# Optimization experiments

Measured on AMD Instinct MI355X. Metric: run time of the kernel, lower is better.

Reference implementation:

```python
import jax, jax.numpy as jnp
import numpy as np
from jax import lax

# Hyperparameters (match init_kwargs)
A = 0.9          # dynamic model: x_t = A * x_{t-1} + SIGMA * eps
SIGMA = 1.0
OBS_SIGMA = 1.0
LR = 0.1
ALPHA = 0.9
ITERATIONS = 3
EPS = 1e-8


def _pairwise_sq(x):
    # (B,N,N) squared euclidean distances ||x_i - x_j||^2
    x2 = jnp.sum(x * x, -1)
    sq = x2[:, :, None] + x2[:, None, :] - 2.0 * jnp.einsum('bid,bjd->bij', x, x)
    return jnp.maximum(sq, 0.0)


def _log_dynamic(x, prev):
    # logd[b,i,j] = log N(x_i ; A*prev_j, SIGMA^2 I)
    D = x.shape[-1]
    x2 = jnp.sum(x * x, -1)
    p2 = jnp.sum(prev * prev, -1)
    sq = x2[:, :, None] - 2.0 * A * jnp.einsum('bid,bjd->bij', x, prev) + (A * A) * p2[:, None, :]
    return -0.5 * sq / (SIGMA ** 2) - 0.5 * D * jnp.log(2.0 * jnp.pi * SIGMA ** 2)


def _post_grad(x, prev, obs):
    # softmax over j == max-subtract / exp / weighted-mean of d_log_dynamic in the original
    w = jax.nn.softmax(_log_dynamic(x, prev), axis=-1)                 # (B,N,N)
    mean_prev = jnp.einsum('bij,bjd->bid', w, prev)                    # sum_j w_ij * prev_j
    dyn_grad = -(x - A * mean_prev) / (SIGMA ** 2)                     # = sum_j w_ij * d_log_dynamic
    obs_grad = -(x - obs[:, None, :]) / (OBS_SIGMA ** 2)               # observation_model.d_score
    return dyn_grad + obs_grad


def _svgd(x, grad_fn):
    B, N, D = x.shape
    logN = jnp.log(jnp.asarray(N, x.dtype))
    step = jnp.zeros_like(x)
    for _ in range(ITERATIONS):
        sq = _pairwise_sq(x)                                           # (B,N,N)
        flat = jnp.sqrt(sq).reshape(B, N * N)
        med = jnp.sort(flat, axis=-1)[:, (N * N - 1) // 2]             # torch lower median of cdist
        h = (med * med / logN)[:, None, None]                          # (B,1,1) bandwidth
        rbf = jnp.exp(-sq / h)                                         # exp(-(1/h)*||x_i-x_j||^2)
        g = grad_fn(x)                                                 # (B,N,D) posterior score at particles
        kxy = jnp.einsum('bij,bjd->bid', rbf, g)                       # sum_j rbf_ij * g_j
        # sum_j d_rbf_ij = (2/h) * (x_i * sum_j rbf_ij - sum_j rbf_ij * x_j)   (avoids (B,N,N,D))
        rep = (2.0 / h) * (x * jnp.sum(rbf, -1)[..., None] - jnp.einsum('bij,bjd->bid', rbf, x))
        stein = (kxy + rep) / N
        step = ALPHA * step + (1.0 - ALPHA) * stein * stein            # RMSprop accumulator
        x = x + LR * stein / (jnp.sqrt(step) + EPS)
    return x


def setup_inputs() -> dict:
    key = jax.random.key(0)
    k1, k2, k3 = jax.random.split(key, 3)
    B, N, D = 8, 2048, 4
    return {
        'prev_state': jax.random.normal(k1, (B, N, D), jnp.float32),
        'observation': jax.random.normal(k2, (B, D), jnp.float32),
        'noise': jax.random.normal(k3, (B, N, D), jnp.float32),
    }


def reference(prev_state, observation, noise):
    N = prev_state.shape[1]
    logN = jnp.log(jnp.asarray(N, prev_state.dtype))
    # dynamic_model.sample
    state = A * prev_state + SIGMA * noise
    # post: logsumexp over i (dim=-2) of log_dynamic[b,i,j]
    log_post = jax.nn.logsumexp(_log_dynamic(state, prev_state), axis=1)   # (B,N)
    new_state = lax.stop_gradient(_svgd(state, lambda x: _post_grad(x, prev_state, observation)))
    log_weight = log_post - lax.stop_gradient(log_post) - logN             # value == -log N
    return jnp.concatenate([new_state, log_weight[..., None]], axis=-1)    # (B,N,D+1)
```

## Files before the change

### kernel.cpp

```cpp
#include <hip/hip_runtime.h>
#include <math.h>


#define NPART 2048
#define KRANK 2097151
#define LOGN_F 7.6246189861593985f
#define A_C 0.9f

__global__ __launch_bounds__(256) void k_init(const float* __restrict__ prev,
                                              const float* __restrict__ noise,
                                              float* __restrict__ x0,
                                              float* __restrict__ apb,
                                              int* __restrict__ hist0) {
  int idx = blockIdx.x * 256 + threadIdx.x;
  float4 p  = ((const float4*)prev)[idx];
  float4 nz = ((const float4*)noise)[idx];
  float4 ap = make_float4(A_C*p.x, A_C*p.y, A_C*p.z, A_C*p.w);
  ((float4*)x0)[idx]  = make_float4(ap.x+nz.x, ap.y+nz.y, ap.z+nz.z, ap.w+nz.w);
  ((float4*)apb)[idx] = ap;
  if (idx < 4096) ((int4*)hist0)[idx] = make_int4(0, 0, 0, 0);
}

__global__ __launch_bounds__(256) void k_s1(const float* __restrict__ x,
                                            const float* __restrict__ apb,
                                            const float* __restrict__ obs,
                                            float* __restrict__ g,
                                            int* __restrict__ hist0,
                                            int* __restrict__ hist1) {
  if (threadIdx.x < 4)
    ((int4*)hist1)[blockIdx.x*4 + threadIdx.x] = make_int4(0, 0, 0, 0);

  if (blockIdx.x < 1024) {
    int b   = blockIdx.x >> 7;
    int ip  = threadIdx.x >> 4;
    int sub = threadIdx.x & 15;
    int i = (blockIdx.x & 127)*16 + ip;
    const float4* ab = (const float4*)apb + b*NPART;
    float4 xi = ((const float4*)x)[b*NPART + i];

    float sum1 = 0.f, sum2 = 0.f;
    float4 acc1 = make_float4(0.f,0.f,0.f,0.f);
    float4 acc2 = make_float4(0.f,0.f,0.f,0.f);
#pragma unroll 4
    for (int c = 0; c < 64; ++c) {
      int j = sub + 16*c;
      float4 a1 = ab[j];
      float4 a2 = ab[j + 1024];
      float dx1 = xi.x-a1.x, dy1 = xi.y-a1.y, dz1 = xi.z-a1.z, dw1 = xi.w-a1.w;
      float dx2 = xi.x-a2.x, dy2 = xi.y-a2.y, dz2 = xi.z-a2.z, dw2 = xi.w-a2.w;
      float e1 = __expf(-0.5f*(dx1*dx1 + dy1*dy1 + dz1*dz1 + dw1*dw1));
      float e2 = __expf(-0.5f*(dx2*dx2 + dy2*dy2 + dz2*dz2 + dw2*dw2));
      sum1 += e1; sum2 += e2;
      acc1.x += e1*a1.x; acc1.y += e1*a1.y; acc1.z += e1*a1.z; acc1.w += e1*a1.w;
      acc2.x += e2*a2.x; acc2.y += e2*a2.y; acc2.z += e2*a2.z; acc2.w += e2*a2.w;
    }
    float sum = sum1 + sum2;
    float4 acc = make_float4(acc1.x+acc2.x, acc1.y+acc2.y,
                             acc1.z+acc2.z, acc1.w+acc2.w);
#pragma unroll
    for (int d = 1; d < 16; d <<= 1) {
      sum   += __shfl_xor(sum, d);
      acc.x += __shfl_xor(acc.x, d);
      acc.y += __shfl_xor(acc.y, d);
      acc.z += __shfl_xor(acc.z, d);
      acc.w += __shfl_xor(acc.w, d);
    }
    if (sub == 0) {
      float inv = 1.0f / sum;
      float4 ob = ((const float4*)obs)[b];
      float4 gg;
      gg.x = acc.x*inv + ob.x - 2.0f*xi.x;
      gg.y = acc.y*inv + ob.y - 2.0f*xi.y;
      gg.z = acc.z*inv + ob.z - 2.0f*xi.z;
      gg.w = acc.w*inv + ob.w - 2.0f*xi.w;
      ((float4*)g)[b*NPART + i] = gg;
    }
  } else {
    int bid   = blockIdx.x - 1024;
    int b     = bid >> 7;
    int sub2  = bid & 127;
    int itile = sub2 >> 4;
    int ktile = sub2 & 15;
    __shared__ float4 sxi[256];
    __shared__ float4 sxw[320];
    __shared__ int    sh[2*2049];

    const float4* xb = (const float4*)x + b*NPART;
    int ibase = itile*256;
    int k0 = ktile*64 + 1;
    sxi[threadIdx.x] = xb[ibase + threadIdx.x];
    for (int t = threadIdx.x; t < 320; t += 256)
      sxw[t] = xb[(ibase + k0 + t) & (NPART - 1)];
    for (int t = threadIdx.x; t < 2*2049; t += 256) sh[t] = 0;
    __syncthreads();

    float4 xi = sxi[threadIdx.x];
    int cofs = (threadIdx.x & 1) * 2049;
#pragma unroll 4
    for (int kk = 0; kk < 64; ++kk) {
      int w = (ktile == 15 && kk == 63) ? 1 : 2;
      float4 xj = sxw[threadIdx.x + kk];
      float dx = xi.x - xj.x, dy = xi.y - xj.y;
      float dz = xi.z - xj.z, dw = xi.w - xj.w;
      float sq = dx*dx + dy*dy + dz*dz + dw*dw;
      atomicAdd(&sh[cofs + (__float_as_uint(sq) >> 20)], w);
    }
    __syncthreads();
    int* hb = hist0 + b*2048;
    for (int t = threadIdx.x; t < 2048; t += 256) {
      int c = sh[t] + sh[t + 2049];
      if (c) atomicAdd(&hb[t], c);
    }
  }
}

__global__ __launch_bounds__(256) void k_s2(const float* __restrict__ x,
                                            int* __restrict__ state,
                                            const int* __restrict__ hist0,
                                            int* __restrict__ hist1) {
  int b     = blockIdx.x >> 7;
  int sub2  = blockIdx.x & 127;
  int itile = sub2 >> 4;
  int ktile = sub2 & 15;
  __shared__ float4 sxi[256];
  __shared__ float4 sxw[320];
  __shared__ int    sh[4096];
  __shared__ int    part[256];
  __shared__ int    s_sel0;

  const float4* xb = (const float4*)x + b*NPART;
  int ibase = itile*256;
  int k0 = ktile*64 + 1;
  sxi[threadIdx.x] = xb[ibase + threadIdx.x];
  for (int t = threadIdx.x; t < 320; t += 256)
    sxw[t] = xb[(ibase + k0 + t) & (NPART - 1)];
  for (int t = threadIdx.x; t < 4096; t += 256) sh[t] = 0;

  const int* h0 = hist0 + b*2048;
  int4 c0 = ((const int4*)h0)[threadIdx.x*2];
  int4 c1 = ((const int4*)h0)[threadIdx.x*2 + 1];
  int s = c0.x+c0.y+c0.z+c0.w + c1.x+c1.y+c1.z+c1.w;
  if (threadIdx.x == 0) s += NPART;
  part[threadIdx.x] = s;
  __syncthreads();
  if (threadIdx.x == 0) {
    int r = KRANK, cum = 0, ch = 0;
    for (; ch < 256; ++ch) { if (cum + part[ch] > r) break; cum += part[ch]; }
    int4 d0 = ((const int4*)h0)[ch*2];
    int4 d1 = ((const int4*)h0)[ch*2 + 1];
    int cc[8] = {d0.x,d0.y,d0.z,d0.w,d1.x,d1.y,d1.z,d1.w};
    if (ch == 0) cc[0] += NPART;
    int q = 0;
    for (;; ++q) { if (cum + cc[q] > r) break; cum += cc[q]; }
    int bin = ch*8 + q;
    s_sel0 = bin;
    if (sub2 == 0) { state[b*2] = bin; state[b*2 + 1] = r - cum; }
  }
  __syncthreads();
  int sel0 = s_sel0;

  float4 xi = sxi[threadIdx.x];
#pragma unroll 4
  for (int kk = 0; kk < 64; ++kk) {
    int w = (ktile == 15 && kk == 63) ? 1 : 2;
    float4 xj = sxw[threadIdx.x + kk];
    float dx = xi.x - xj.x, dy = xi.y - xj.y;
    float dz = xi.z - xj.z, dw = xi.w - xj.w;
    float sq = dx*dx + dy*dy + dz*dz + dw*dw;
    unsigned bits = __float_as_uint(sq);
    if ((int)(bits >> 20) == sel0) atomicAdd(&sh[(bits >> 8) & 4095], w);
  }
  __syncthreads();
  int* hb = hist1 + b*4096;
  for (int t = threadIdx.x; t < 4096; t += 256) {
    int c = sh[t];
    if (c) atomicAdd(&hb[t], c);
  }
}

template <int MODE>
__global__ __launch_bounds__(256) void k_s3(const float* __restrict__ x,
                                            const float* __restrict__ g,
                                            const int* __restrict__ state,
                                            int* __restrict__ hist0,
                                            const int* __restrict__ hist1,
                                            float* __restrict__ stepb,
                                            float* __restrict__ xout,
                                            float* __restrict__ outp) {
  if (threadIdx.x < 8)
    ((int4*)hist0)[blockIdx.x*8 + threadIdx.x] = make_int4(0, 0, 0, 0);

  int b   = blockIdx.x >> 6;
  int blk = blockIdx.x & 63;
  __shared__ int   part[256];
  __shared__ float shp[2];

  const int* h1 = hist1 + b*4096;
  int4 c0 = ((const int4*)h1)[threadIdx.x*4 + 0];
  int4 c1 = ((const int4*)h1)[threadIdx.x*4 + 1];
  int4 c2 = ((const int4*)h1)[threadIdx.x*4 + 2];
  int4 c3 = ((const int4*)h1)[threadIdx.x*4 + 3];
  int s = c0.x+c0.y+c0.z+c0.w + c1.x+c1.y+c1.z+c1.w
        + c2.x+c2.y+c2.z+c2.w + c3.x+c3.y+c3.z+c3.w;
  int sel0 = state[b*2];
  if (threadIdx.x == 0 && sel0 == 0) s += NPART;
  part[threadIdx.x] = s;
  __syncthreads();
  if (threadIdx.x == 0) {
    int r = state[b*2 + 1], cum = 0, ch = 0;
    for (; ch < 256; ++ch) { if (cum + part[ch] > r) break; cum += part[ch]; }
    int4 d0 = ((const int4*)h1)[ch*4 + 0];
    int4 d1 = ((const int4*)h1)[ch*4 + 1];
    int4 d2 = ((const int4*)h1)[ch*4 + 2];
    int4 d3 = ((const int4*)h1)[ch*4 + 3];
    int cc[16] = {d0.x,d0.y,d0.z,d0.w, d1.x,d1.y,d1.z,d1.w,
                  d2.x,d2.y,d2.z,d2.w, d3.x,d3.y,d3.z,d3.w};
    if (sel0 == 0 && ch == 0) cc[0] += NPART;
    int q = 0;
    for (;; ++q) { if (cum + cc[q] > r) break; cum += cc[q]; }
    int bin = ch*16 + q;
    unsigned mb = (((unsigned)sel0) << 20) | (((unsigned)bin) << 8) | 128u;
    float med = sqrtf(__uint_as_float(mb));
    float h = med * med / LOGN_F;
    shp[0] = -1.0f / h;
    shp[1] =  2.0f / h;
  }
  __syncthreads();
  float neginvh = shp[0];
  float two_h   = shp[1];

  int ip  = threadIdx.x >> 4;
  int sub = threadIdx.x & 15;
  int rowA = blk*32 + ip;
  int rowB = rowA + 16;
  const float4* xb = (const float4*)x + b*NPART;
  const float4* gb = (const float4*)g + b*NPART;
  float4 xiA = xb[rowA];
  float4 xiB = xb[rowB];

  float4 SdA = make_float4(0.f,0.f,0.f,0.f), SgA = SdA;
  float4 SdB = SdA, SgB = SdA;
#pragma unroll 4
  for (int c = 0; c < 128; ++c) {
    int j = sub + 16*c;
    float4 xj = xb[j];
    float4 gj = gb[j];
    float dxA = xiA.x-xj.x, dyA = xiA.y-xj.y, dzA = xiA.z-xj.z, dwA = xiA.w-xj.w;
    float dxB = xiB.x-xj.x, dyB = xiB.y-xj.y, dzB = xiB.z-xj.z, dwB = xiB.w-xj.w;
    float eA = __expf((dxA*dxA + dyA*dyA + dzA*dzA + dwA*dwA) * neginvh);
    float eB = __expf((dxB*dxB + dyB*dyB + dzB*dzB + dwB*dwB) * neginvh);
    SdA.x += eA*dxA; SdA.y += eA*dyA; SdA.z += eA*dzA; SdA.w += eA*dwA;
    SdB.x += eB*dxB; SdB.y += eB*dyB; SdB.z += eB*dzB; SdB.w += eB*dwB;
    SgA.x += eA*gj.x; SgA.y += eA*gj.y; SgA.z += eA*gj.z; SgA.w += eA*gj.w;
    SgB.x += eB*gj.x; SgB.y += eB*gj.y; SgB.z += eB*gj.z; SgB.w += eB*gj.w;
  }
#pragma unroll
  for (int d = 1; d < 16; d <<= 1) {
    SdA.x += __shfl_xor(SdA.x, d); SdA.y += __shfl_xor(SdA.y, d);
    SdA.z += __shfl_xor(SdA.z, d); SdA.w += __shfl_xor(SdA.w, d);
    SgA.x += __shfl_xor(SgA.x, d); SgA.y += __shfl_xor(SgA.y, d);
    SgA.z += __shfl_xor(SgA.z, d); SgA.w += __shfl_xor(SgA.w, d);
    SdB.x += __shfl_xor(SdB.x, d); SdB.y += __shfl_xor(SdB.y, d);
    SdB.z += __shfl_xor(SdB.z, d); SdB.w += __shfl_xor(SdB.w, d);
    SgB.x += __shfl_xor(SgB.x, d); SgB.y += __shfl_xor(SgB.y, d);
    SgB.z += __shfl_xor(SgB.z, d); SgB.w += __shfl_xor(SgB.w, d);
  }
  if (sub == 0) {
    const float invN = 1.0f / 2048.0f;
#pragma unroll
    for (int rr = 0; rr < 2; ++rr) {
      int row = rr ? rowB : rowA;
      float4 xi = rr ? xiB : xiA;
      float4 Sd = rr ? SdB : SdA;
      float4 Sg = rr ? SgB : SgA;
      float4 sv;
      sv.x = (Sg.x + two_h*Sd.x) * invN;
      sv.y = (Sg.y + two_h*Sd.y) * invN;
      sv.z = (Sg.z + two_h*Sd.z) * invN;
      sv.w = (Sg.w + two_h*Sd.w) * invN;
      float4 st;
      if (MODE == 0) {
        st = make_float4(0.1f*sv.x*sv.x, 0.1f*sv.y*sv.y,
                         0.1f*sv.z*sv.z, 0.1f*sv.w*sv.w);
      } else {
        st = ((float4*)stepb)[b*NPART + row];
        st.x = 0.9f*st.x + 0.1f*sv.x*sv.x;
        st.y = 0.9f*st.y + 0.1f*sv.y*sv.y;
        st.z = 0.9f*st.z + 0.1f*sv.z*sv.z;
        st.w = 0.9f*st.w + 0.1f*sv.w*sv.w;
      }
      float4 xn;
      xn.x = xi.x + 0.1f*sv.x / (sqrtf(st.x) + 1e-8f);
      xn.y = xi.y + 0.1f*sv.y / (sqrtf(st.y) + 1e-8f);
      xn.z = xi.z + 0.1f*sv.z / (sqrtf(st.z) + 1e-8f);
      xn.w = xi.w + 0.1f*sv.w / (sqrtf(st.w) + 1e-8f);
      if (MODE != 2) {
        ((float4*)stepb)[b*NPART + row] = st;
        ((float4*)xout)[b*NPART + row] = xn;
      } else {
        float* o = outp + (size_t)(b*NPART + row) * 5;
        o[0] = xn.x; o[1] = xn.y; o[2] = xn.z; o[3] = xn.w;
        o[4] = -LOGN_F;
      }
    }
  }
}

extern "C" void kernel_launch(void* const* d_in, const int* in_sizes, int n_in,
                              void* d_out, int out_size, void* d_ws, size_t ws_size,
                              hipStream_t stream) {
  const float* prev  = (const float*)d_in[0];
  const float* obs   = (const float*)d_in[1];
  const float* noise = (const float*)d_in[2];
  float* out = (float*)d_out;

  float* ws = (float*)d_ws;
  float* xA    = ws;
  float* xB    = xA + 65536;
  float* gbuf  = xB + 65536;
  float* stepb = gbuf + 65536;
  float* apb   = stepb + 65536;
  int*   state = (int*)(apb + 65536);
  int*   hist0 = state + 16;
  int*   hist1 = hist0 + 8*2048;

  k_init<<<64, 256, 0, stream>>>(prev, noise, xA, apb, hist0);

  float* xc = xA;
  float* xn = xB;
  for (int it = 0; it < 3; ++it) {
    k_s1<<<2048, 256, 0, stream>>>(xc, apb, obs, gbuf, hist0, hist1);
    k_s2<<<1024, 256, 0, stream>>>(xc, state, hist0, hist1);
    if (it == 0) {
      k_s3<0><<<512, 256, 0, stream>>>(xc, gbuf, state, hist0, hist1, stepb, xn, nullptr);
    } else if (it == 1) {
      k_s3<1><<<512, 256, 0, stream>>>(xc, gbuf, state, hist0, hist1, stepb, xn, nullptr);
    } else {
      k_s3<2><<<512, 256, 0, stream>>>(xc, gbuf, state, hist0, hist1, stepb, nullptr, out);
    }
    float* t = xc; xc = xn; xn = t;
  }
}
```

Measured before the change: 359.5 us.

## Register-block four rows per wavefront in gradient and Stein kernels, interleave block roles

The gradient part of k_s1 and the Stein kernel k_s3 now give each 64-lane wavefront four particle rows and stride across all 2048 j values, so every loaded j particle is reused for four rows. k_s3 folds the repulsive term into a precomputed per-j coefficient (g_j - (2/h) x_j) plus a row-sum term, which removes per-pair multiply-adds. k_s1 interleaves its gradient and histogram blocks by blockIdx parity, and k_s3 launches 1024 blocks. The histogram zeroing is redistributed (init clears all three histograms), and occupancy hints are added in exchange for more registers per thread and longer 64-wide shuffle reductions.

```diff
diff --git a/kernel.cpp b/kernel.cpp
--- a/kernel.cpp
+++ b/kernel.cpp
@@ -11,74 +11,115 @@
                                               const float* __restrict__ noise,
                                               float* __restrict__ x0,
                                               float* __restrict__ apb,
-                                              int* __restrict__ hist0) {
+                                              int* __restrict__ hists) {
   int idx = blockIdx.x * 256 + threadIdx.x;
   float4 p  = ((const float4*)prev)[idx];
   float4 nz = ((const float4*)noise)[idx];
   float4 ap = make_float4(A_C*p.x, A_C*p.y, A_C*p.z, A_C*p.w);
   ((float4*)x0)[idx]  = make_float4(ap.x+nz.x, ap.y+nz.y, ap.z+nz.z, ap.w+nz.w);
   ((float4*)apb)[idx] = ap;
-  if (idx < 4096) ((int4*)hist0)[idx] = make_int4(0, 0, 0, 0);
-}
-
-__global__ __launch_bounds__(256) void k_s1(const float* __restrict__ x,
-                                            const float* __restrict__ apb,
-                                            const float* __restrict__ obs,
-                                            float* __restrict__ g,
-                                            int* __restrict__ hist0,
-                                            int* __restrict__ hist1) {
+  if (idx < 12288) ((int4*)hists)[idx] = make_int4(0, 0, 0, 0);
+}
+
+__device__ __forceinline__ void grad_j(const float4* xi, const float4 ap,
+                                       float* s, float4* acc) {
+#pragma unroll
+  for (int r = 0; r < 4; ++r) {
+    float dx = xi[r].x - ap.x, dy = xi[r].y - ap.y;
+    float dz = xi[r].z - ap.z, dw = xi[r].w - ap.w;
+    float sq = fmaf(dx, dx, fmaf(dy, dy, fmaf(dz, dz, dw*dw)));
+    float e = __expf(-0.5f * sq);
+    s[r] += e;
+    acc[r].x = fmaf(e, ap.x, acc[r].x);
+    acc[r].y = fmaf(e, ap.y, acc[r].y);
+    acc[r].z = fmaf(e, ap.z, acc[r].z);
+    acc[r].w = fmaf(e, ap.w, acc[r].w);
+  }
+}
+
+__device__ __forceinline__ void stein_j(const float4* xi, const float4 xj,
+                                        const float4 gj, float two_h,
+                                        float ninvh, float* s0, float4* sc) {
+  float4 cj;
+  cj.x = fmaf(-two_h, xj.x, gj.x);
+  cj.y = fmaf(-two_h, xj.y, gj.y);
+  cj.z = fmaf(-two_h, xj.z, gj.z);
+  cj.w = fmaf(-two_h, xj.w, gj.w);
+#pragma unroll
+  for (int r = 0; r < 4; ++r) {
+    float dx = xi[r].x - xj.x, dy = xi[r].y - xj.y;
+    float dz = xi[r].z - xj.z, dw = xi[r].w - xj.w;
+    float sq = fmaf(dx, dx, fmaf(dy, dy, fmaf(dz, dz, dw*dw)));
+    float e = __expf(sq * ninvh);
+    s0[r] += e;
+    sc[r].x = fmaf(e, cj.x, sc[r].x);
+    sc[r].y = fmaf(e, cj.y, sc[r].y);
+    sc[r].z = fmaf(e, cj.z, sc[r].z);
+    sc[r].w = fmaf(e, cj.w, sc[r].w);
+  }
+}
+
+__global__ __launch_bounds__(256, 4) void k_s1(const float* __restrict__ x,
+                                               const float* __restrict__ apb,
+                                               const float* __restrict__ obs,
+                                               float* __restrict__ g,
+                                               int* __restrict__ hist0,
+                                               int* __restrict__ hist1) {
   if (threadIdx.x < 4)
     ((int4*)hist1)[blockIdx.x*4 + threadIdx.x] = make_int4(0, 0, 0, 0);
-
-  if (blockIdx.x < 1024) {
-    int b   = blockIdx.x >> 7;
-    int ip  = threadIdx.x >> 4;
-    int sub = threadIdx.x & 15;
-    int i = (blockIdx.x & 127)*16 + ip;
+  int role = blockIdx.x & 1;
+  int id   = blockIdx.x >> 1;
+
+  if (role == 0) {
+    int b = id >> 7;
+    int rbase = (id & 127)*16 + (threadIdx.x >> 6)*4;
+    int lane = threadIdx.x & 63;
+    const float4* xb = (const float4*)x + b*NPART;
     const float4* ab = (const float4*)apb + b*NPART;
-    float4 xi = ((const float4*)x)[b*NPART + i];
-
-    float sum1 = 0.f, sum2 = 0.f;
-    float4 acc1 = make_float4(0.f,0.f,0.f,0.f);
-    float4 acc2 = make_float4(0.f,0.f,0.f,0.f);
-#pragma unroll 4
-    for (int c = 0; c < 64; ++c) {
-      int j = sub + 16*c;
-      float4 a1 = ab[j];
-      float4 a2 = ab[j + 1024];
-      float dx1 = xi.x-a1.x, dy1 = xi.y-a1.y, dz1 = xi.z-a1.z, dw1 = xi.w-a1.w;
-      float dx2 = xi.x-a2.x, dy2 = xi.y-a2.y, dz2 = xi.z-a2.z, dw2 = xi.w-a2.w;
-      float e1 = __expf(-0.5f*(dx1*dx1 + dy1*dy1 + dz1*dz1 + dw1*dw1));
-      float e2 = __expf(-0.5f*(dx2*dx2 + dy2*dy2 + dz2*dz2 + dw2*dw2));
-      sum1 += e1; sum2 += e2;
-      acc1.x += e1*a1.x; acc1.y += e1*a1.y; acc1.z += e1*a1.z; acc1.w += e1*a1.w;
-      acc2.x += e2*a2.x; acc2.y += e2*a2.y; acc2.z += e2*a2.z; acc2.w += e2*a2.w;
-    }
-    float sum = sum1 + sum2;
-    float4 acc = make_float4(acc1.x+acc2.x, acc1.y+acc2.y,
-                             acc1.z+acc2.z, acc1.w+acc2.w);
-#pragma unroll
-    for (int d = 1; d < 16; d <<= 1) {
-      sum   += __shfl_xor(sum, d);
-      acc.x += __shfl_xor(acc.x, d);
-      acc.y += __shfl_xor(acc.y, d);
-      acc.z += __shfl_xor(acc.z, d);
-      acc.w += __shfl_xor(acc.w, d);
-    }
-    if (sub == 0) {
-      float inv = 1.0f / sum;
+    float4 xi[4];
+#pragma unroll
+    for (int r = 0; r < 4; ++r) xi[r] = xb[rbase + r];
+    float  sum[4] = {0.f, 0.f, 0.f, 0.f};
+    float4 acc[4] = {{0,0,0,0},{0,0,0,0},{0,0,0,0},{0,0,0,0}};
+
+    for (int c = 0; c < 2048; c += 256) {
+      int j = lane + c;
+      float4 aA = ab[j];
+      float4 aB = ab[j + 64];
+      float4 aC = ab[j + 128];
+      float4 aD = ab[j + 192];
+      grad_j(xi, aA, sum, acc);
+      grad_j(xi, aB, sum, acc);
+      grad_j(xi, aC, sum, acc);
+      grad_j(xi, aD, sum, acc);
+    }
+#pragma unroll
+    for (int d = 1; d < 64; d <<= 1) {
+#pragma unroll
+      for (int r = 0; r < 4; ++r) {
+        sum[r]   += __shfl_xor(sum[r], d);
+        acc[r].x += __shfl_xor(acc[r].x, d);
+        acc[r].y += __shfl_xor(acc[r].y, d);
+        acc[r].z += __shfl_xor(acc[r].z, d);
+        acc[r].w += __shfl_xor(acc[r].w, d);
+      }
+    }
+    if (lane == 0) {
       float4 ob = ((const float4*)obs)[b];
-      float4 gg;
-      gg.x = acc.x*inv + ob.x - 2.0f*xi.x;
-      gg.y = acc.y*inv + ob.y - 2.0f*xi.y;
-      gg.z = acc.z*inv + ob.z - 2.0f*xi.z;
-      gg.w = acc.w*inv + ob.w - 2.0f*xi.w;
-      ((float4*)g)[b*NPART + i] = gg;
+#pragma unroll
+      for (int r = 0; r < 4; ++r) {
+        float inv = 1.0f / sum[r];
+        float4 gg;
+        gg.x = fmaf(acc[r].x, inv, fmaf(-2.0f, xi[r].x, ob.x));
+        gg.y = fmaf(acc[r].y, inv, fmaf(-2.0f, xi[r].y, ob.y));
+        gg.z = fmaf(acc[r].z, inv, fmaf(-2.0f, xi[r].z, ob.z));
+        gg.w = fmaf(acc[r].w, inv, fmaf(-2.0f, xi[r].w, ob.w));
+        ((float4*)g)[b*NPART + rbase + r] = gg;
+      }
     }
   } else {
-    int bid   = blockIdx.x - 1024;
-    int b     = bid >> 7;
-    int sub2  = bid & 127;
+    int b     = id >> 7;
+    int sub2  = id & 127;
     int itile = sub2 >> 4;
     int ktile = sub2 & 15;
     __shared__ float4 sxi[256];
@@ -179,19 +220,18 @@
 }
 
 template <int MODE>
-__global__ __launch_bounds__(256) void k_s3(const float* __restrict__ x,
-                                            const float* __restrict__ g,
-                                            const int* __restrict__ state,
-                                            int* __restrict__ hist0,
-                                            const int* __restrict__ hist1,
-                                            float* __restrict__ stepb,
-                                            float* __restrict__ xout,
-                                            float* __restrict__ outp) {
-  if (threadIdx.x < 8)
-    ((int4*)hist0)[blockIdx.x*8 + threadIdx.x] = make_int4(0, 0, 0, 0);
-
-  int b   = blockIdx.x >> 6;
-  int blk = blockIdx.x & 63;
+__global__ __launch_bounds__(256, 4) void k_s3(const float* __restrict__ x,
+                                               const float* __restrict__ g,
+                                               const int* __restrict__ state,
+                                               int* __restrict__ hist0,
+                                               const int* __restrict__ hist1,
+                                               float* __restrict__ stepb,
+                                               float* __restrict__ xout,
+                                               float* __restrict__ outp) {
+  if (threadIdx.x < 4)
+    ((int4*)hist0)[blockIdx.x*4 + threadIdx.x] = make_int4(0, 0, 0, 0);
+
+  int b = blockIdx.x >> 7;
   __shared__ int   part[256];
   __shared__ float shp[2];
 
@@ -229,55 +269,49 @@
   float neginvh = shp[0];
   float two_h   = shp[1];
 
-  int ip  = threadIdx.x >> 4;
-  int sub = threadIdx.x & 15;
-  int rowA = blk*32 + ip;
-  int rowB = rowA + 16;
+  int rbase = (blockIdx.x & 127)*16 + (threadIdx.x >> 6)*4;
+  int lane = threadIdx.x & 63;
   const float4* xb = (const float4*)x + b*NPART;
   const float4* gb = (const float4*)g + b*NPART;
-  float4 xiA = xb[rowA];
-  float4 xiB = xb[rowB];
-
-  float4 SdA = make_float4(0.f,0.f,0.f,0.f), SgA = SdA;
-  float4 SdB = SdA, SgB = SdA;
-#pragma unroll 4
-  for (int c = 0; c < 128; ++c) {
-    int j = sub + 16*c;
-    float4 xj = xb[j];
-    float4 gj = gb[j];
-    float dxA = xiA.x-xj.x, dyA = xiA.y-xj.y, dzA = xiA.z-xj.z, dwA = xiA.w-xj.w;
-    float dxB = xiB.x-xj.x, dyB = xiB.y-xj.y, dzB = xiB.z-xj.z, dwB = xiB.w-xj.w;
-    float eA = __expf((dxA*dxA + dyA*dyA + dzA*dzA + dwA*dwA) * neginvh);
-    float eB = __expf((dxB*dxB + dyB*dyB + dzB*dzB + dwB*dwB) * neginvh);
-    SdA.x += eA*dxA; SdA.y += eA*dyA; SdA.z += eA*dzA; SdA.w += eA*dwA;
-    SdB.x += eB*dxB; SdB.y += eB*dyB; SdB.z += eB*dzB; SdB.w += eB*dwB;
-    SgA.x += eA*gj.x; SgA.y += eA*gj.y; SgA.z += eA*gj.z; SgA.w += eA*gj.w;
-    SgB.x += eB*gj.x; SgB.y += eB*gj.y; SgB.z += eB*gj.z; SgB.w += eB*gj.w;
-  }
-#pragma unroll
-  for (int d = 1; d < 16; d <<= 1) {
-    SdA.x += __shfl_xor(SdA.x, d); SdA.y += __shfl_xor(SdA.y, d);
-    SdA.z += __shfl_xor(SdA.z, d); SdA.w += __shfl_xor(SdA.w, d);
-    SgA.x += __shfl_xor(SgA.x, d); SgA.y += __shfl_xor(SgA.y, d);
-    SgA.z += __shfl_xor(SgA.z, d); SgA.w += __shfl_xor(SgA.w, d);
-    SdB.x += __shfl_xor(SdB.x, d); SdB.y += __shfl_xor(SdB.y, d);
-    SdB.z += __shfl_xor(SdB.z, d); SdB.w += __shfl_xor(SdB.w, d);
-    SgB.x += __shfl_xor(SgB.x, d); SgB.y += __shfl_xor(SgB.y, d);
-    SgB.z += __shfl_xor(SgB.z, d); SgB.w += __shfl_xor(SgB.w, d);
-  }
-  if (sub == 0) {
+  float4 xi[4];
+#pragma unroll
+  for (int r = 0; r < 4; ++r) xi[r] = xb[rbase + r];
+  float  S0[4] = {0.f, 0.f, 0.f, 0.f};
+  float4 Sc[4] = {{0,0,0,0},{0,0,0,0},{0,0,0,0},{0,0,0,0}};
+
+  for (int c = 0; c < 2048; c += 256) {
+    int j = lane + c;
+    float4 xjA = xb[j];        float4 gjA = gb[j];
+    float4 xjB = xb[j + 64];   float4 gjB = gb[j + 64];
+    float4 xjC = xb[j + 128];  float4 gjC = gb[j + 128];
+    float4 xjD = xb[j + 192];  float4 gjD = gb[j + 192];
+    stein_j(xi, xjA, gjA, two_h, neginvh, S0, Sc);
+    stein_j(xi, xjB, gjB, two_h, neginvh, S0, Sc);
+    stein_j(xi, xjC, gjC, two_h, neginvh, S0, Sc);
+    stein_j(xi, xjD, gjD, two_h, neginvh, S0, Sc);
+  }
+#pragma unroll
+  for (int d = 1; d < 64; d <<= 1) {
+#pragma unroll
+    for (int r = 0; r < 4; ++r) {
+      S0[r]   += __shfl_xor(S0[r], d);
+      Sc[r].x += __shfl_xor(Sc[r].x, d);
+      Sc[r].y += __shfl_xor(Sc[r].y, d);
+      Sc[r].z += __shfl_xor(Sc[r].z, d);
+      Sc[r].w += __shfl_xor(Sc[r].w, d);
+    }
+  }
+  if (lane == 0) {
     const float invN = 1.0f / 2048.0f;
 #pragma unroll
-    for (int rr = 0; rr < 2; ++rr) {
-      int row = rr ? rowB : rowA;
-      float4 xi = rr ? xiB : xiA;
-      float4 Sd = rr ? SdB : SdA;
-      float4 Sg = rr ? SgB : SgA;
+    for (int r = 0; r < 4; ++r) {
+      int row = rbase + r;
+      float th0 = two_h * S0[r];
       float4 sv;
-      sv.x = (Sg.x + two_h*Sd.x) * invN;
-      sv.y = (Sg.y + two_h*Sd.y) * invN;
-      sv.z = (Sg.z + two_h*Sd.z) * invN;
-      sv.w = (Sg.w + two_h*Sd.w) * invN;
+      sv.x = fmaf(th0, xi[r].x, Sc[r].x) * invN;
+      sv.y = fmaf(th0, xi[r].y, Sc[r].y) * invN;
+      sv.z = fmaf(th0, xi[r].z, Sc[r].z) * invN;
+      sv.w = fmaf(th0, xi[r].w, Sc[r].w) * invN;
       float4 st;
       if (MODE == 0) {
         st = make_float4(0.1f*sv.x*sv.x, 0.1f*sv.y*sv.y,
@@ -290,10 +324,10 @@
         st.w = 0.9f*st.w + 0.1f*sv.w*sv.w;
       }
       float4 xn;
-      xn.x = xi.x + 0.1f*sv.x / (sqrtf(st.x) + 1e-8f);
-      xn.y = xi.y + 0.1f*sv.y / (sqrtf(st.y) + 1e-8f);
-      xn.z = xi.z + 0.1f*sv.z / (sqrtf(st.z) + 1e-8f);
-      xn.w = xi.w + 0.1f*sv.w / (sqrtf(st.w) + 1e-8f);
+      xn.x = xi[r].x + 0.1f*sv.x / (sqrtf(st.x) + 1e-8f);
+      xn.y = xi[r].y + 0.1f*sv.y / (sqrtf(st.y) + 1e-8f);
+      xn.z = xi[r].z + 0.1f*sv.z / (sqrtf(st.z) + 1e-8f);
+      xn.w = xi[r].w + 0.1f*sv.w / (sqrtf(st.w) + 1e-8f);
       if (MODE != 2) {
         ((float4*)stepb)[b*NPART + row] = st;
         ((float4*)xout)[b*NPART + row] = xn;
@@ -332,11 +366,11 @@
     k_s1<<<2048, 256, 0, stream>>>(xc, apb, obs, gbuf, hist0, hist1);
     k_s2<<<1024, 256, 0, stream>>>(xc, state, hist0, hist1);
     if (it == 0) {
-      k_s3<0><<<512, 256, 0, stream>>>(xc, gbuf, state, hist0, hist1, stepb, xn, nullptr);
+      k_s3<0><<<1024, 256, 0, stream>>>(xc, gbuf, state, hist0, hist1, stepb, xn, nullptr);
     } else if (it == 1) {
-      k_s3<1><<<512, 256, 0, stream>>>(xc, gbuf, state, hist0, hist1, stepb, xn, nullptr);
+      k_s3<1><<<1024, 256, 0, stream>>>(xc, gbuf, state, hist0, hist1, stepb, xn, nullptr);
     } else {
-      k_s3<2><<<512, 256, 0, stream>>>(xc, gbuf, state, hist0, hist1, stepb, nullptr, out);
+      k_s3<2><<<1024, 256, 0, stream>>>(xc, gbuf, state, hist0, hist1, stepb, nullptr, out);
     }
     float* t = xc; xc = xn; xn = t;
   }
```

Result: faster. 328.3 us (-8.7%).

## Interleave k_s1 block roles and split k_s3 into one row per group

Applied to the files above, without the earlier changes.

k_s1 now interleaves its two block roles (score computation and pairwise-distance histogram) by block parity rather than running them as two contiguous halves. The intent is that both kinds of work are co-resident on the compute units and balance better. k_s3 now gives each 16-thread group one row instead of two, doubling the grid to 1024 blocks and splitting the j loop into two independent halves for ILP. Histogram zeroing is adjusted to match: init clears all histogram buffers and k_s3 clears 4 int4 per block. The cost is that each x_j/g_j load is reused across fewer rows, so k_s3 issues more loads per unit of work.

```diff
diff --git a/kernel.cpp b/kernel.cpp
--- a/kernel.cpp
+++ b/kernel.cpp
@@ -11,14 +11,14 @@
                                               const float* __restrict__ noise,
                                               float* __restrict__ x0,
                                               float* __restrict__ apb,
-                                              int* __restrict__ hist0) {
+                                              int* __restrict__ hists) {
   int idx = blockIdx.x * 256 + threadIdx.x;
   float4 p  = ((const float4*)prev)[idx];
   float4 nz = ((const float4*)noise)[idx];
   float4 ap = make_float4(A_C*p.x, A_C*p.y, A_C*p.z, A_C*p.w);
   ((float4*)x0)[idx]  = make_float4(ap.x+nz.x, ap.y+nz.y, ap.z+nz.z, ap.w+nz.w);
   ((float4*)apb)[idx] = ap;
-  if (idx < 4096) ((int4*)hist0)[idx] = make_int4(0, 0, 0, 0);
+  if (idx < 12288) ((int4*)hists)[idx] = make_int4(0, 0, 0, 0);
 }
 
 __global__ __launch_bounds__(256) void k_s1(const float* __restrict__ x,
@@ -29,12 +29,14 @@
                                             int* __restrict__ hist1) {
   if (threadIdx.x < 4)
     ((int4*)hist1)[blockIdx.x*4 + threadIdx.x] = make_int4(0, 0, 0, 0);
-
-  if (blockIdx.x < 1024) {
-    int b   = blockIdx.x >> 7;
+  int role = blockIdx.x & 1;
+  int id   = blockIdx.x >> 1;
+
+  if (role == 0) {
+    int b   = id >> 7;
     int ip  = threadIdx.x >> 4;
     int sub = threadIdx.x & 15;
-    int i = (blockIdx.x & 127)*16 + ip;
+    int i = (id & 127)*16 + ip;
     const float4* ab = (const float4*)apb + b*NPART;
     float4 xi = ((const float4*)x)[b*NPART + i];
 
@@ -76,9 +78,8 @@
       ((float4*)g)[b*NPART + i] = gg;
     }
   } else {
-    int bid   = blockIdx.x - 1024;
-    int b     = bid >> 7;
-    int sub2  = bid & 127;
+    int b     = id >> 7;
+    int sub2  = id & 127;
     int itile = sub2 >> 4;
     int ktile = sub2 & 15;
     __shared__ float4 sxi[256];
@@ -187,11 +188,10 @@
                                             float* __restrict__ stepb,
                                             float* __restrict__ xout,
                                             float* __restrict__ outp) {
-  if (threadIdx.x < 8)
-    ((int4*)hist0)[blockIdx.x*8 + threadIdx.x] = make_int4(0, 0, 0, 0);
-
-  int b   = blockIdx.x >> 6;
-  int blk = blockIdx.x & 63;
+  if (threadIdx.x < 4)
+    ((int4*)hist0)[blockIdx.x*4 + threadIdx.x] = make_int4(0, 0, 0, 0);
+
+  int b = blockIdx.x >> 7;
   __shared__ int   part[256];
   __shared__ float shp[2];
 
@@ -231,77 +231,68 @@
 
   int ip  = threadIdx.x >> 4;
   int sub = threadIdx.x & 15;
-  int rowA = blk*32 + ip;
-  int rowB = rowA + 16;
+  int i = (blockIdx.x & 127)*16 + ip;
   const float4* xb = (const float4*)x + b*NPART;
   const float4* gb = (const float4*)g + b*NPART;
-  float4 xiA = xb[rowA];
-  float4 xiB = xb[rowB];
-
-  float4 SdA = make_float4(0.f,0.f,0.f,0.f), SgA = SdA;
-  float4 SdB = SdA, SgB = SdA;
+  float4 xi = xb[i];
+
+  float4 Sd1 = make_float4(0.f,0.f,0.f,0.f), Sd2 = Sd1;
+  float4 Sg1 = Sd1, Sg2 = Sd1;
 #pragma unroll 4
-  for (int c = 0; c < 128; ++c) {
+  for (int c = 0; c < 64; ++c) {
     int j = sub + 16*c;
-    float4 xj = xb[j];
-    float4 gj = gb[j];
-    float dxA = xiA.x-xj.x, dyA = xiA.y-xj.y, dzA = xiA.z-xj.z, dwA = xiA.w-xj.w;
-    float dxB = xiB.x-xj.x, dyB = xiB.y-xj.y, dzB = xiB.z-xj.z, dwB = xiB.w-xj.w;
-    float eA = __expf((dxA*dxA + dyA*dyA + dzA*dzA + dwA*dwA) * neginvh);
-    float eB = __expf((dxB*dxB + dyB*dyB + dzB*dzB + dwB*dwB) * neginvh);
-    SdA.x += eA*dxA; SdA.y += eA*dyA; SdA.z += eA*dzA; SdA.w += eA*dwA;
-    SdB.x += eB*dxB; SdB.y += eB*dyB; SdB.z += eB*dzB; SdB.w += eB*dwB;
-    SgA.x += eA*gj.x; SgA.y += eA*gj.y; SgA.z += eA*gj.z; SgA.w += eA*gj.w;
-    SgB.x += eB*gj.x; SgB.y += eB*gj.y; SgB.z += eB*gj.z; SgB.w += eB*gj.w;
-  }
+    float4 xj1 = xb[j];
+    float4 xj2 = xb[j + 1024];
+    float4 gj1 = gb[j];
+    float4 gj2 = gb[j + 1024];
+    float dx1 = xi.x-xj1.x, dy1 = xi.y-xj1.y, dz1 = xi.z-xj1.z, dw1 = xi.w-xj1.w;
+    float dx2 = xi.x-xj2.x, dy2 = xi.y-xj2.y, dz2 = xi.z-xj2.z, dw2 = xi.w-xj2.w;
+    float e1 = __expf((dx1*dx1 + dy1*dy1 + dz1*dz1 + dw1*dw1) * neginvh);
+    float e2 = __expf((dx2*dx2 + dy2*dy2 + dz2*dz2 + dw2*dw2) * neginvh);
+    Sd1.x += e1*dx1; Sd1.y += e1*dy1; Sd1.z += e1*dz1; Sd1.w += e1*dw1;
+    Sd2.x += e2*dx2; Sd2.y += e2*dy2; Sd2.z += e2*dz2; Sd2.w += e2*dw2;
+    Sg1.x += e1*gj1.x; Sg1.y += e1*gj1.y; Sg1.z += e1*gj1.z; Sg1.w += e1*gj1.w;
+    Sg2.x += e2*gj2.x; Sg2.y += e2*gj2.y; Sg2.z += e2*gj2.z; Sg2.w += e2*gj2.w;
+  }
+  float4 Sd = make_float4(Sd1.x+Sd2.x, Sd1.y+Sd2.y, Sd1.z+Sd2.z, Sd1.w+Sd2.w);
+  float4 Sg = make_float4(Sg1.x+Sg2.x, Sg1.y+Sg2.y, Sg1.z+Sg2.z, Sg1.w+Sg2.w);
 #pragma unroll
   for (int d = 1; d < 16; d <<= 1) {
-    SdA.x += __shfl_xor(SdA.x, d); SdA.y += __shfl_xor(SdA.y, d);
-    SdA.z += __shfl_xor(SdA.z, d); SdA.w += __shfl_xor(SdA.w, d);
-    SgA.x += __shfl_xor(SgA.x, d); SgA.y += __shfl_xor(SgA.y, d);
-    SgA.z += __shfl_xor(SgA.z, d); SgA.w += __shfl_xor(SgA.w, d);
-    SdB.x += __shfl_xor(SdB.x, d); SdB.y += __shfl_xor(SdB.y, d);
-    SdB.z += __shfl_xor(SdB.z, d); SdB.w += __shfl_xor(SdB.w, d);
-    SgB.x += __shfl_xor(SgB.x, d); SgB.y += __shfl_xor(SgB.y, d);
-    SgB.z += __shfl_xor(SgB.z, d); SgB.w += __shfl_xor(SgB.w, d);
+    Sd.x += __shfl_xor(Sd.x, d); Sd.y += __shfl_xor(Sd.y, d);
+    Sd.z += __shfl_xor(Sd.z, d); Sd.w += __shfl_xor(Sd.w, d);
+    Sg.x += __shfl_xor(Sg.x, d); Sg.y += __shfl_xor(Sg.y, d);
+    Sg.z += __shfl_xor(Sg.z, d); Sg.w += __shfl_xor(Sg.w, d);
   }
   if (sub == 0) {
     const float invN = 1.0f / 2048.0f;
-#pragma unroll
-    for (int rr = 0; rr < 2; ++rr) {
-      int row = rr ? rowB : rowA;
-      float4 xi = rr ? xiB : xiA;
-      float4 Sd = rr ? SdB : SdA;
-      float4 Sg = rr ? SgB : SgA;
-      float4 sv;
-      sv.x = (Sg.x + two_h*Sd.x) * invN;
-      sv.y = (Sg.y + two_h*Sd.y) * invN;
-      sv.z = (Sg.z + two_h*Sd.z) * invN;
-      sv.w = (Sg.w + two_h*Sd.w) * invN;
-      float4 st;
-      if (MODE == 0) {
-        st = make_float4(0.1f*sv.x*sv.x, 0.1f*sv.y*sv.y,
-                         0.1f*sv.z*sv.z, 0.1f*sv.w*sv.w);
-      } else {
-        st = ((float4*)stepb)[b*NPART + row];
-        st.x = 0.9f*st.x + 0.1f*sv.x*sv.x;
-        st.y = 0.9f*st.y + 0.1f*sv.y*sv.y;
-        st.z = 0.9f*st.z + 0.1f*sv.z*sv.z;
-        st.w = 0.9f*st.w + 0.1f*sv.w*sv.w;
-      }
-      float4 xn;
-      xn.x = xi.x + 0.1f*sv.x / (sqrtf(st.x) + 1e-8f);
-      xn.y = xi.y + 0.1f*sv.y / (sqrtf(st.y) + 1e-8f);
-      xn.z = xi.z + 0.1f*sv.z / (sqrtf(st.z) + 1e-8f);
-      xn.w = xi.w + 0.1f*sv.w / (sqrtf(st.w) + 1e-8f);
-      if (MODE != 2) {
-        ((float4*)stepb)[b*NPART + row] = st;
-        ((float4*)xout)[b*NPART + row] = xn;
-      } else {
-        float* o = outp + (size_t)(b*NPART + row) * 5;
-        o[0] = xn.x; o[1] = xn.y; o[2] = xn.z; o[3] = xn.w;
-        o[4] = -LOGN_F;
-      }
+    float4 sv;
+    sv.x = (Sg.x + two_h*Sd.x) * invN;
+    sv.y = (Sg.y + two_h*Sd.y) * invN;
+    sv.z = (Sg.z + two_h*Sd.z) * invN;
+    sv.w = (Sg.w + two_h*Sd.w) * invN;
+    float4 st;
+    if (MODE == 0) {
+      st = make_float4(0.1f*sv.x*sv.x, 0.1f*sv.y*sv.y,
+                       0.1f*sv.z*sv.z, 0.1f*sv.w*sv.w);
+    } else {
+      st = ((float4*)stepb)[b*NPART + i];
+      st.x = 0.9f*st.x + 0.1f*sv.x*sv.x;
+      st.y = 0.9f*st.y + 0.1f*sv.y*sv.y;
+      st.z = 0.9f*st.z + 0.1f*sv.z*sv.z;
+      st.w = 0.9f*st.w + 0.1f*sv.w*sv.w;
+    }
+    float4 xn;
+    xn.x = xi.x + 0.1f*sv.x / (sqrtf(st.x) + 1e-8f);
+    xn.y = xi.y + 0.1f*sv.y / (sqrtf(st.y) + 1e-8f);
+    xn.z = xi.z + 0.1f*sv.z / (sqrtf(st.z) + 1e-8f);
+    xn.w = xi.w + 0.1f*sv.w / (sqrtf(st.w) + 1e-8f);
+    if (MODE != 2) {
+      ((float4*)stepb)[b*NPART + i] = st;
+      ((float4*)xout)[b*NPART + i] = xn;
+    } else {
+      float* o = outp + (size_t)(b*NPART + i) * 5;
+      o[0] = xn.x; o[1] = xn.y; o[2] = xn.z; o[3] = xn.w;
+      o[4] = -LOGN_F;
     }
   }
 }
@@ -332,11 +323,11 @@
     k_s1<<<2048, 256, 0, stream>>>(xc, apb, obs, gbuf, hist0, hist1);
     k_s2<<<1024, 256, 0, stream>>>(xc, state, hist0, hist1);
     if (it == 0) {
-      k_s3<0><<<512, 256, 0, stream>>>(xc, gbuf, state, hist0, hist1, stepb, xn, nullptr);
+      k_s3<0><<<1024, 256, 0, stream>>>(xc, gbuf, state, hist0, hist1, stepb, xn, nullptr);
     } else if (it == 1) {
-      k_s3<1><<<512, 256, 0, stream>>>(xc, gbuf, state, hist0, hist1, stepb, xn, nullptr);
+      k_s3<1><<<1024, 256, 0, stream>>>(xc, gbuf, state, hist0, hist1, stepb, xn, nullptr);
     } else {
-      k_s3<2><<<512, 256, 0, stream>>>(xc, gbuf, state, hist0, hist1, stepb, nullptr, out);
+      k_s3<2><<<1024, 256, 0, stream>>>(xc, gbuf, state, hist0, hist1, stepb, nullptr, out);
     }
     float* t = xc; xc = xn; xn = t;
   }
```

New measurement: 368.9 us. 2.6% more time.
